# Optimization experiments

Hardware: AMD Instinct MI355X
Metric: run time of the kernel (lower is better)

The kernel has to match this reference:

```python
import jax, jax.numpy as jnp
import numpy as np

B, S, D, H, DH, BS, L, R, V, FF = 4, 4096, 768, 12, 64, 64, 2, 3, 50257, 3072
NB = S // BS          # 64 key/query blocks
NSEL = 5 + R          # 2 global + 3 window + R random key blocks per query block


def layer_norm(x, g, b, eps=1e-12):
    m = jnp.mean(x, axis=-1, keepdims=True)
    v = jnp.mean(jnp.square(x - m), axis=-1, keepdims=True)
    return (x - m) * jax.lax.rsqrt(v + eps) * g + b


def setup_inputs() -> dict:
    key = jax.random.key(0)
    ks = iter(jax.random.split(key, 16))
    p = lambda shape: jax.random.normal(next(ks), shape, jnp.float32) * 0.02
    return {
        'input_ids': jax.random.randint(next(ks), (B, S), 0, V, jnp.int32),
        'attention_mask': jnp.ones((B, S), jnp.int32),
        'label': jax.random.randint(next(ks), (B,), 0, 2, jnp.int32),
        'rand_idx': jax.random.randint(next(ks), (NB, R), 0, NB, jnp.int32),
        'emb': p((V, D)), 'pos_emb': p((S, D)),
        'ln_emb_g': jnp.ones((D,)), 'ln_emb_b': jnp.zeros((D,)),
        'Wqkv': p((L, D, 3 * D)), 'bqkv': jnp.zeros((L, 3 * D)),
        'Wo': p((L, D, D)), 'bo': jnp.zeros((L, D)),
        'ln1_g': jnp.ones((L, D)), 'ln1_b': jnp.zeros((L, D)),
        'Wff1': p((L, D, FF)), 'bff1': jnp.zeros((L, FF)),
        'Wff2': p((L, FF, D)), 'bff2': jnp.zeros((L, D)),
        'ln2_g': jnp.ones((L, D)), 'ln2_b': jnp.zeros((L, D)),
        'Wp': p((D, D)), 'bp': jnp.zeros((D,)),
        'Wc': p((D, 2)), 'bc': jnp.zeros((2,)),
    }


def reference(input_ids, attention_mask, label, rand_idx, emb, pos_emb,
              ln_emb_g, ln_emb_b, Wqkv, bqkv, Wo, bo, ln1_g, ln1_b,
              Wff1, bff1, Wff2, bff2, ln2_g, ln2_b, Wp, bp, Wc, bc):
    blk = jnp.arange(NB, dtype=jnp.int32)
    sel = jnp.concatenate([
        jnp.zeros((NB, 1), jnp.int32),
        ((blk - 1) % NB)[:, None], blk[:, None], ((blk + 1) % NB)[:, None],
        jnp.full((NB, 1), NB - 1, jnp.int32),
        rand_idx.astype(jnp.int32),
    ], axis=1)  # [NB, NSEL]

    h = emb[input_ids] + pos_emb[None]                 # [B,S,D]
    h = layer_norm(h, ln_emb_g, ln_emb_b)

    mblk = attention_mask.reshape(B, NB, BS)
    mask_sel = mblk[:, sel].reshape(B, 1, NB, 1, NSEL * BS)  # gathered key mask
    bias = jnp.where(mask_sel > 0, 0.0, -1e9).astype(h.dtype)

    scale = 1.0 / np.sqrt(DH)
    for l in range(L):
        qkv = h @ Wqkv[l] + bqkv[l]
        q, k, v = jnp.split(qkv, 3, axis=-1)
        to_blocks = lambda t: t.reshape(B, NB, BS, H, DH).transpose(0, 3, 1, 2, 4)  # [B,H,NB,BS,DH]
        qb, kb, vb = to_blocks(q), to_blocks(k), to_blocks(v)
        ksel = kb[:, :, sel].reshape(B, H, NB, NSEL * BS, DH)  # gather sparse key blocks
        vsel = vb[:, :, sel].reshape(B, H, NB, NSEL * BS, DH)
        scores = jnp.einsum('bhnqd,bhnkd->bhnqk', qb, ksel) * scale + bias
        attn = jax.nn.softmax(scores, axis=-1)
        ob = jnp.einsum('bhnqk,bhnkd->bhnqd', attn, vsel)
        o = ob.transpose(0, 2, 3, 1, 4).reshape(B, S, D)
        h = layer_norm(h + o @ Wo[l] + bo[l], ln1_g[l], ln1_b[l])
        ff = jax.nn.gelu(h @ Wff1[l] + bff1[l]) @ Wff2[l] + bff2[l]
        h = layer_norm(h + ff, ln2_g[l], ln2_b[l])

    pooled = jnp.tanh(h[:, 0] @ Wp + bp)               # BERT-style pooler on [CLS]
    probs = jax.nn.softmax(pooled @ Wc + bc, axis=1)
    # Faithful to the original: CrossEntropyLoss applied to softmax OUTPUT (double softmax)
    loss = -jnp.mean(jax.nn.log_softmax(probs, axis=1)[jnp.arange(B), label])
    return probs, loss
```

## Files before the change

kernel.cpp:

```cpp
#include <hip/hip_runtime.h>
#include <hip/hip_bf16.h>
#include <stdint.h>


using bf16 = __hip_bfloat16;
typedef __bf16 bf16x8 __attribute__((ext_vector_type(8)));
typedef float f32x4 __attribute__((ext_vector_type(4)));

__device__ __forceinline__ float b2f(bf16 x) { return __bfloat162float(x); }
__device__ __forceinline__ bf16 f2b(float x) { return __float2bfloat16(x); }
__device__ __forceinline__ float ldf(const void* p, size_t i, int flag) {
  return flag ? __bfloat162float(((const bf16*)p)[i]) : ((const float*)p)[i];
}

__device__ __forceinline__ void gld_lds16(const bf16* g, bf16* l) {
  __builtin_amdgcn_global_load_lds((__attribute__((address_space(1))) void*)g,
                                   (__attribute__((address_space(3))) void*)l, 16, 0, 0);
}

__device__ __forceinline__ f32x4 mfma16(bf16x8 a, bf16x8 b, f32x4 c) {
  return __builtin_amdgcn_mfma_f32_16x16x32_bf16(a, b, c, 0, 0, 0);
}

__global__ void probe_kernel(const uint32_t* __restrict__ g, int* __restrict__ flag) {
  if (threadIdx.x == 0) flag[0] = (g[0] == 0x3F803F80u) ? 1 : 0;
}

__global__ __launch_bounds__(256) void transpose_k(const void* __restrict__ in, size_t in_off,
                                                   bf16* __restrict__ out, int K, int N,
                                                   const int* __restrict__ dflag) {
  __shared__ float tile[32][33];
  const int flag = dflag[0];
  const int bx = blockIdx.x * 32;
  const int by = blockIdx.y * 32;
  const int tx = threadIdx.x & 31, ty = threadIdx.x >> 5;
#pragma unroll
  for (int i = 0; i < 32; i += 8)
    tile[ty + i][tx] = ldf(in, in_off + (size_t)(by + ty + i) * N + bx + tx, flag);
  __syncthreads();
#pragma unroll
  for (int i = 0; i < 32; i += 8)
    out[(size_t)(bx + ty + i) * K + by + tx] = f2b(tile[tx][ty + i]);
}

__global__ __launch_bounds__(256) void embed_ln_kernel(
    const int* __restrict__ ids, const void* __restrict__ emb, const void* __restrict__ pos,
    const void* __restrict__ g, const void* __restrict__ bb, bf16* __restrict__ h,
    const int* __restrict__ dflag) {
  __shared__ float red[8];
  const int flag = dflag[0];
  const int tok = blockIdx.x;
  const int tid = threadIdx.x;
  const int s = tok & 4095;
  const size_t id = (size_t)ids[tok];
  float v[3]; float sum = 0.f, sq = 0.f;
#pragma unroll
  for (int i = 0; i < 3; i++) {
    const int d = tid + i * 256;
    v[i] = ldf(emb, id * 768 + d, flag) + ldf(pos, (size_t)s * 768 + d, flag);
    sum += v[i]; sq += v[i] * v[i];
  }
#pragma unroll
  for (int off = 32; off >= 1; off >>= 1) { sum += __shfl_down(sum, off); sq += __shfl_down(sq, off); }
  if ((tid & 63) == 0) { red[(tid >> 6) * 2] = sum; red[(tid >> 6) * 2 + 1] = sq; }
  __syncthreads();
  sum = red[0] + red[2] + red[4] + red[6];
  sq  = red[1] + red[3] + red[5] + red[7];
  const float mean = sum * (1.0f / 768.0f);
  const float var = sq * (1.0f / 768.0f) - mean * mean;
  const float rs = rsqrtf(var + 1e-12f);
  bf16* hr = h + (size_t)tok * 768;
#pragma unroll
  for (int i = 0; i < 3; i++) {
    const int d = tid + i * 256;
    hr[d] = f2b((v[i] - mean) * rs * ldf(g, d, flag) + ldf(bb, d, flag));
  }
}

__global__ __launch_bounds__(256) void add_ln_kernel(
    bf16* __restrict__ h, const bf16* __restrict__ x,
    const void* __restrict__ g, const void* __restrict__ bb, size_t goff,
    const int* __restrict__ dflag) {
  __shared__ float red[8];
  const int flag = dflag[0];
  const int tok = blockIdx.x;
  const int tid = threadIdx.x;
  const size_t base = (size_t)tok * 768;
  float v[3]; float sum = 0.f, sq = 0.f;
#pragma unroll
  for (int i = 0; i < 3; i++) {
    const int d = tid + i * 256;
    v[i] = b2f(h[base + d]) + b2f(x[base + d]);
    sum += v[i]; sq += v[i] * v[i];
  }
#pragma unroll
  for (int off = 32; off >= 1; off >>= 1) { sum += __shfl_down(sum, off); sq += __shfl_down(sq, off); }
  if ((tid & 63) == 0) { red[(tid >> 6) * 2] = sum; red[(tid >> 6) * 2 + 1] = sq; }
  __syncthreads();
  sum = red[0] + red[2] + red[4] + red[6];
  sq  = red[1] + red[3] + red[5] + red[7];
  const float mean = sum * (1.0f / 768.0f);
  const float var = sq * (1.0f / 768.0f) - mean * mean;
  const float rs = rsqrtf(var + 1e-12f);
#pragma unroll
  for (int i = 0; i < 3; i++) {
    const int d = tid + i * 256;
    h[base + d] = f2b((v[i] - mean) * rs * ldf(g, goff + d, flag) + ldf(bb, goff + d, flag));
  }
}

template <int EPI, bool ABLK>
__global__ __launch_bounds__(256) void gemm_bt(
    const bf16* __restrict__ A, const bf16* __restrict__ Bt,
    const void* __restrict__ bias, size_t bias_off, bf16* __restrict__ C,
    int N, int K,
    bf16* __restrict__ qout, bf16* __restrict__ kout, bf16* __restrict__ vout,
    const int* __restrict__ dflag) {
  __shared__ __align__(16) bf16 sA[128 * 32];
  __shared__ __align__(16) bf16 sB[128 * 32];
  const int m0 = blockIdx.x * 128;
  const int n0 = blockIdx.y * 128;
  const int tid = threadIdx.x;
  const int lane = tid & 63;
  const int wv = tid >> 6;
  const int wm = wv >> 1, wn = wv & 1;
  const int col = lane & 15, quad = lane >> 4;

  f32x4 acc[4][4] = {};

  const int sr = tid >> 2;
  const int sc = (tid & 3) * 8;
  const bf16* gA = A + (size_t)(m0 + sr) * K + sc;
  const bf16* gB = Bt + (size_t)(n0 + sr) * K + sc;
  const size_t rstep = (size_t)64 * K;

  size_t cb0 = 0, cb1 = 0;
  if constexpr (ABLK) {
    const int t0 = m0 + sr, t1 = t0 + 64;
    cb0 = (size_t)(t0 >> 12) * 3145728 + ((t0 >> 6) & 63) * 4096 + (t0 & 63) * 64;
    cb1 = (size_t)(t1 >> 12) * 3145728 + ((t1 >> 6) & 63) * 4096 + (t1 & 63) * 64;
  }

  for (int k0 = 0; k0 < K; k0 += 32) {
    const bf16 *pA0, *pA1;
    if constexpr (ABLK) {
      const int c = k0 + sc;
      const int hh = c >> 6, dh = c & 63;
      pA0 = A + cb0 + hh * 262144 + dh;
      pA1 = A + cb1 + hh * 262144 + dh;
    } else {
      pA0 = gA; pA1 = gA + rstep; gA += 32;
    }
    gld_lds16(pA0, sA + tid * 8);
    gld_lds16(pA1, sA + 2048 + tid * 8);
    gld_lds16(gB, sB + tid * 8);
    gld_lds16(gB + rstep, sB + 2048 + tid * 8);
    gB += 32;
    __syncthreads();
    bf16x8 av[4], bv[4];
#pragma unroll
    for (int t = 0; t < 4; t++)
      av[t] = *(const bf16x8*)(sA + (wm * 64 + t * 16 + col) * 32 + quad * 8);
#pragma unroll
    for (int t = 0; t < 4; t++)
      bv[t] = *(const bf16x8*)(sB + (wn * 64 + t * 16 + col) * 32 + quad * 8);
#pragma unroll
    for (int mt = 0; mt < 4; mt++)
#pragma unroll
      for (int nt = 0; nt < 4; nt++)
        acc[mt][nt] = mfma16(av[mt], bv[nt], acc[mt][nt]);
    __syncthreads();
  }

  const int flag = dflag[0];
#pragma unroll
  for (int nt = 0; nt < 4; nt++) {
    const int n = n0 + wn * 64 + nt * 16 + col;
    const float bsv = ldf(bias, bias_off + n, flag);
#pragma unroll
    for (int mt = 0; mt < 4; mt++) {
#pragma unroll
      for (int r = 0; r < 4; r++) {
        const int m = m0 + wm * 64 + mt * 16 + quad * 4 + r;
        float val = acc[mt][nt][r] + bsv;
        if constexpr (EPI == 1) {
          val = 0.5f * val * (1.0f + tanhf(0.7978845608028654f * (val + 0.044715f * val * val * val)));
        }
        if constexpr (EPI == 2) {
          const int part = (n >= 1536) ? 2 : ((n >= 768) ? 1 : 0);
          const int within = n - part * 768;
          const int hh = within >> 6, dh = within & 63;
          const int bb = m >> 12;
          const int nb = (m >> 6) & 63, pos = m & 63;
          const size_t base = (size_t)((bb * 12 + hh) * 64 + nb) * 4096;
          if (part == 0)      qout[base + pos * 64 + dh] = f2b(val);
          else if (part == 1) kout[base + pos * 64 + dh] = f2b(val);
          else                vout[base + dh * 64 + pos] = f2b(val);
        } else {
          C[(size_t)m * N + n] = f2b(val);
        }
      }
    }
  }
}

__global__ __launch_bounds__(256) void attn_kernel(
    const bf16* q, const bf16* __restrict__ kmat, const bf16* __restrict__ vT,
    const int* __restrict__ amask, const int* __restrict__ rand_idx, bf16* o) {
  __shared__ __align__(16) bf16 plds[4][16][32];
  const int idx = blockIdx.x;
  const int nb = idx & 63;
  const int bh = idx >> 6;
  const int bb = bh / 12;
  const int tid = threadIdx.x;
  const int wv = tid >> 6, lane = tid & 63;
  const int col = lane & 15, quad = lane >> 4;

  int sel[8];
  sel[0] = 0; sel[1] = (nb + 63) & 63; sel[2] = nb; sel[3] = (nb + 1) & 63;
  sel[4] = 63;
  sel[5] = rand_idx[nb * 3 + 0];
  sel[6] = rand_idx[nb * 3 + 1];
  sel[7] = rand_idx[nb * 3 + 2];

  const size_t bhbase = (size_t)bh * 64;
  const bf16* qb = q + (bhbase + nb) * 4096;
  const int qrow = wv * 16 + col;
  const bf16x8 aq0 = *(const bf16x8*)(qb + qrow * 64 + quad * 8);
  const bf16x8 aq1 = *(const bf16x8*)(qb + qrow * 64 + 32 + quad * 8);

  float sreg[32][4];
#pragma unroll
  for (int sb = 0; sb < 8; sb++) {
    const bf16* kb = kmat + (bhbase + sel[sb]) * 4096;
    const int* mrow = amask + bb * 4096 + sel[sb] * 64;
#pragma unroll
    for (int c = 0; c < 4; c++) {
      const int kr = c * 16 + col;
      const bf16x8 bk0 = *(const bf16x8*)(kb + kr * 64 + quad * 8);
      const bf16x8 bk1 = *(const bf16x8*)(kb + kr * 64 + 32 + quad * 8);
      f32x4 t = {};
      t = mfma16(aq0, bk0, t);
      t = mfma16(aq1, bk1, t);
      const float bias = (mrow[kr] > 0) ? 0.0f : -1e9f;
      const int ti = sb * 4 + c;
#pragma unroll
      for (int r = 0; r < 4; r++) sreg[ti][r] = t[r] * 0.125f + bias;
    }
  }

  float mx[4] = {-1e30f, -1e30f, -1e30f, -1e30f};
#pragma unroll
  for (int ti = 0; ti < 32; ti++)
#pragma unroll
    for (int r = 0; r < 4; r++) mx[r] = fmaxf(mx[r], sreg[ti][r]);
#pragma unroll
  for (int off = 8; off >= 1; off >>= 1)
#pragma unroll
    for (int r = 0; r < 4; r++) mx[r] = fmaxf(mx[r], __shfl_xor(mx[r], off));

  float sm[4] = {0.f, 0.f, 0.f, 0.f};
#pragma unroll
  for (int ti = 0; ti < 32; ti++)
#pragma unroll
    for (int r = 0; r < 4; r++) {
      const float p = __expf(sreg[ti][r] - mx[r]);
      sreg[ti][r] = p; sm[r] += p;
    }
#pragma unroll
  for (int off = 8; off >= 1; off >>= 1)
#pragma unroll
    for (int r = 0; r < 4; r++) sm[r] += __shfl_xor(sm[r], off);
  float inv[4];
#pragma unroll
  for (int r = 0; r < 4; r++) inv[r] = 1.0f / sm[r];

  f32x4 oacc[4] = {};
#pragma unroll
  for (int kc = 0; kc < 16; kc++) {
    __syncthreads();
#pragma unroll
    for (int j = 0; j < 2; j++)
#pragma unroll
      for (int r = 0; r < 4; r++)
        plds[wv][quad * 4 + r][j * 16 + col] = f2b(sreg[kc * 2 + j][r] * inv[r]);
    __syncthreads();
    const bf16x8 ap = *(const bf16x8*)(&plds[wv][col][quad * 8]);
    const int sb = kc >> 1;
    const int koff = (kc & 1) * 32 + quad * 8;
    const bf16* vb = vT + (bhbase + sel[sb]) * 4096;
#pragma unroll
    for (int nt = 0; nt < 4; nt++) {
      const bf16x8 bvv = *(const bf16x8*)(vb + (nt * 16 + col) * 64 + koff);
      oacc[nt] = mfma16(ap, bvv, oacc[nt]);
    }
  }

  bf16* ob = o + (bhbase + nb) * 4096;
#pragma unroll
  for (int nt = 0; nt < 4; nt++)
#pragma unroll
    for (int r = 0; r < 4; r++)
      ob[(wv * 16 + quad * 4 + r) * 64 + nt * 16 + col] = f2b(oacc[nt][r]);
}

__global__ __launch_bounds__(768) void pooler_kernel(
    const bf16* __restrict__ h, const void* __restrict__ Wp,
    const void* __restrict__ bp, float* __restrict__ pooled,
    const int* __restrict__ dflag) {
  __shared__ float hrow[768];
  const int flag = dflag[0];
  const int bb = blockIdx.x;
  const int j = threadIdx.x;
  hrow[j] = b2f(h[(size_t)bb * 4096 * 768 + j]);
  __syncthreads();
  float acc = 0.0f;
#pragma unroll 8
  for (int d = 0; d < 768; d++) acc += hrow[d] * ldf(Wp, (size_t)d * 768 + j, flag);
  pooled[bb * 768 + j] = tanhf(acc + ldf(bp, j, flag));
}

__global__ __launch_bounds__(256) void cls_kernel(
    const float* __restrict__ pooled, const void* __restrict__ Wc, const void* __restrict__ bc,
    const int* __restrict__ label, void* __restrict__ out, const int* __restrict__ dflag) {
  __shared__ float lsum[8];
  const int flag = dflag[0];
  const int tid = threadIdx.x;
  const int p = tid >> 5, i = tid & 31;
  const int bb = p >> 1, c = p & 1;
  float acc = 0.0f;
  for (int d = i; d < 768; d += 32) acc += pooled[bb * 768 + d] * ldf(Wc, (size_t)d * 2 + c, flag);
#pragma unroll
  for (int off = 16; off >= 1; off >>= 1) acc += __shfl_xor(acc, off);
  if (i == 0) lsum[p] = acc;
  __syncthreads();
  if (tid == 0) {
    float res[9];
    float loss = 0.0f;
    for (int b = 0; b < 4; b++) {
      const float l0 = lsum[b * 2 + 0] + ldf(bc, 0, flag);
      const float l1 = lsum[b * 2 + 1] + ldf(bc, 1, flag);
      const float m = fmaxf(l0, l1);
      const float e0 = expf(l0 - m), e1 = expf(l1 - m);
      const float s = e0 + e1;
      const float p0 = e0 / s, p1 = e1 / s;
      res[b * 2] = p0; res[b * 2 + 1] = p1;
      const float mm = fmaxf(p0, p1);
      const float lse = mm + logf(expf(p0 - mm) + expf(p1 - mm));
      const float chosen = (label[b] == 0) ? p0 : p1;
      loss -= (chosen - lse);
    }
    res[8] = loss * 0.25f;
    if (flag) { bf16* o = (bf16*)out; for (int j = 0; j < 9; j++) o[j] = f2b(res[j]); }
    else      { float* o = (float*)out; for (int j = 0; j < 9; j++) o[j] = res[j]; }
  }
}

extern "C" void kernel_launch(void* const* d_in, const int* in_sizes, int n_in,
                              void* d_out, int out_size, void* d_ws, size_t ws_size,
                              hipStream_t stream) {
  const int* input_ids      = (const int*)d_in[0];
  const int* attention_mask = (const int*)d_in[1];
  const int* label          = (const int*)d_in[2];
  const int* rand_idx       = (const int*)d_in[3];
  const void* emb      = d_in[4];
  const void* pos_emb  = d_in[5];
  const void* ln_emb_g = d_in[6];
  const void* ln_emb_b = d_in[7];
  const void* Wqkv = d_in[8];
  const void* bqkv = d_in[9];
  const void* Wo   = d_in[10];
  const void* bo   = d_in[11];
  const void* ln1_g = d_in[12];
  const void* ln1_b = d_in[13];
  const void* Wff1 = d_in[14];
  const void* bff1 = d_in[15];
  const void* Wff2 = d_in[16];
  const void* bff2 = d_in[17];
  const void* ln2_g = d_in[18];
  const void* ln2_b = d_in[19];
  const void* Wp = d_in[20];
  const void* bp = d_in[21];
  const void* Wc = d_in[22];
  const void* bc = d_in[23];

  bf16* ws = (bf16*)d_ws;
  size_t off = 0;
  int* dflag = (int*)(ws + off); off += 8;
  bf16* WqkvT = ws + off; off += (size_t)2 * 2304 * 768;
  bf16* WoT   = ws + off; off += (size_t)2 * 768 * 768;
  bf16* Wff1T = ws + off; off += (size_t)2 * 3072 * 768;
  bf16* Wff2T = ws + off; off += (size_t)2 * 768 * 3072;
  bf16* hbuf  = ws + off; off += (size_t)16384 * 768;
  bf16* qo    = ws + off; off += (size_t)16384 * 768;
  bf16* kbf   = ws + off; off += (size_t)16384 * 768;
  bf16* vbf   = ws + off; off += (size_t)16384 * 768;
  bf16* xbf   = ws + off; off += (size_t)16384 * 768;
  bf16* a1buf = ws + off; off += (size_t)16384 * 3072;
  float* pooled = (float*)(ws + off); off += 6144;

  dim3 blk(256);

  probe_kernel<<<1, 64, 0, stream>>>((const uint32_t*)ln_emb_g, dflag);

  for (int l = 0; l < 2; l++) {
    transpose_k<<<dim3(72, 24), blk, 0, stream>>>(Wqkv, (size_t)l * 768 * 2304, WqkvT + (size_t)l * 2304 * 768, 768, 2304, dflag);
    transpose_k<<<dim3(24, 24), blk, 0, stream>>>(Wo, (size_t)l * 768 * 768, WoT + (size_t)l * 768 * 768, 768, 768, dflag);
    transpose_k<<<dim3(96, 24), blk, 0, stream>>>(Wff1, (size_t)l * 768 * 3072, Wff1T + (size_t)l * 3072 * 768, 768, 3072, dflag);
    transpose_k<<<dim3(24, 96), blk, 0, stream>>>(Wff2, (size_t)l * 3072 * 768, Wff2T + (size_t)l * 768 * 3072, 3072, 768, dflag);
  }

  embed_ln_kernel<<<16384, blk, 0, stream>>>(input_ids, emb, pos_emb, ln_emb_g, ln_emb_b, hbuf, dflag);

  for (int l = 0; l < 2; l++) {
    gemm_bt<2, false><<<dim3(128, 18), blk, 0, stream>>>(hbuf, WqkvT + (size_t)l * 2304 * 768, bqkv, (size_t)l * 2304,
                                                         nullptr, 2304, 768, qo, kbf, vbf, dflag);
    attn_kernel<<<3072, blk, 0, stream>>>(qo, kbf, vbf, attention_mask, rand_idx, qo);
    gemm_bt<0, true><<<dim3(128, 6), blk, 0, stream>>>(qo, WoT + (size_t)l * 768 * 768, bo, (size_t)l * 768,
                                                       xbf, 768, 768, nullptr, nullptr, nullptr, dflag);
    add_ln_kernel<<<16384, blk, 0, stream>>>(hbuf, xbf, ln1_g, ln1_b, (size_t)l * 768, dflag);
    gemm_bt<1, false><<<dim3(128, 24), blk, 0, stream>>>(hbuf, Wff1T + (size_t)l * 3072 * 768, bff1, (size_t)l * 3072,
                                                         a1buf, 3072, 768, nullptr, nullptr, nullptr, dflag);
    gemm_bt<0, false><<<dim3(128, 6), blk, 0, stream>>>(a1buf, Wff2T + (size_t)l * 768 * 3072, bff2, (size_t)l * 768,
                                                        xbf, 768, 3072, nullptr, nullptr, nullptr, dflag);
    add_ln_kernel<<<16384, blk, 0, stream>>>(hbuf, xbf, ln2_g, ln2_b, (size_t)l * 768, dflag);
  }

  pooler_kernel<<<4, dim3(768), 0, stream>>>(hbuf, Wp, bp, pooled, dflag);
  cls_kernel<<<1, blk, 0, stream>>>(pooled, Wc, bc, label, d_out, dflag);

  (void)in_sizes; (void)n_in; (void)out_size; (void)ws_size;
}
```

Baseline: 1.863 ms.

## Swizzle GEMM LDS layout and stage epilogue through shared memory for vector stores

Applies an XOR-style rotation to the K-chunk placement in LDS so MFMA operand reads hit distinct banks. Reworks the GEMM epilogue to write each 64-row half of the tile into padded shared memory, then emit 16-byte coalesced global stores, including for the QKV-to-block-layout scatter and the transposed V. It also replaces the tanh-based GELU with an equivalent sigmoid/exp form. The cost is extra barriers and a larger shared-memory footprint per block.

```diff
diff --git a/kernel.cpp b/kernel.cpp
--- a/kernel.cpp
+++ b/kernel.cpp
@@ -5,6 +5,7 @@
 
 using bf16 = __hip_bfloat16;
 typedef __bf16 bf16x8 __attribute__((ext_vector_type(8)));
+typedef __bf16 bf16x4 __attribute__((ext_vector_type(4)));
 typedef float f32x4 __attribute__((ext_vector_type(4)));
 
 __device__ __forceinline__ float b2f(bf16 x) { return __bfloat162float(x); }
@@ -20,6 +21,11 @@
 
 __device__ __forceinline__ f32x4 mfma16(bf16x8 a, bf16x8 b, f32x4 c) {
   return __builtin_amdgcn_mfma_f32_16x16x32_bf16(a, b, c, 0, 0, 0);
+}
+
+__device__ __forceinline__ float gelu_f(float x) {
+  const float z = 1.5957691216057308f * (x + 0.044715f * x * x * x);
+  return x / (1.0f + __expf(-z));
 }
 
 __global__ void probe_kernel(const uint32_t* __restrict__ g, int* __restrict__ flag) {
@@ -116,8 +122,9 @@
     int N, int K,
     bf16* __restrict__ qout, bf16* __restrict__ kout, bf16* __restrict__ vout,
     const int* __restrict__ dflag) {
-  __shared__ __align__(16) bf16 sA[128 * 32];
-  __shared__ __align__(16) bf16 sB[128 * 32];
+  __shared__ __align__(16) bf16 smem[9216];
+  bf16* sA = smem;
+  bf16* sB = smem + 4096;
   const int m0 = blockIdx.x * 128;
   const int n0 = blockIdx.y * 128;
   const int tid = threadIdx.x;
@@ -129,7 +136,8 @@
   f32x4 acc[4][4] = {};
 
   const int sr = tid >> 2;
-  const int sc = (tid & 3) * 8;
+  const int kc = ((tid & 3) - ((tid >> 4) & 3)) & 3;
+  const int sc = kc * 8;
   const bf16* gA = A + (size_t)(m0 + sr) * K + sc;
   const bf16* gB = Bt + (size_t)(n0 + sr) * K + sc;
   const size_t rstep = (size_t)64 * K;
@@ -140,6 +148,8 @@
     cb0 = (size_t)(t0 >> 12) * 3145728 + ((t0 >> 6) & 63) * 4096 + (t0 & 63) * 64;
     cb1 = (size_t)(t1 >> 12) * 3145728 + ((t1 >> 6) & 63) * 4096 + (t1 & 63) * 64;
   }
+
+  const int sl = (quad + (col >> 2)) & 3;
 
   for (int k0 = 0; k0 < K; k0 += 32) {
     const bf16 *pA0, *pA1;
@@ -160,10 +170,10 @@
     bf16x8 av[4], bv[4];
 #pragma unroll
     for (int t = 0; t < 4; t++)
-      av[t] = *(const bf16x8*)(sA + (wm * 64 + t * 16 + col) * 32 + quad * 8);
+      av[t] = *(const bf16x8*)(sA + (wm * 64 + t * 16 + col) * 32 + sl * 8);
 #pragma unroll
     for (int t = 0; t < 4; t++)
-      bv[t] = *(const bf16x8*)(sB + (wn * 64 + t * 16 + col) * 32 + quad * 8);
+      bv[t] = *(const bf16x8*)(sB + (wn * 64 + t * 16 + col) * 32 + sl * 8);
 #pragma unroll
     for (int mt = 0; mt < 4; mt++)
 #pragma unroll
@@ -173,31 +183,86 @@
   }
 
   const int flag = dflag[0];
-#pragma unroll
-  for (int nt = 0; nt < 4; nt++) {
-    const int n = n0 + wn * 64 + nt * 16 + col;
-    const float bsv = ldf(bias, bias_off + n, flag);
-#pragma unroll
-    for (int mt = 0; mt < 4; mt++) {
-#pragma unroll
-      for (int r = 0; r < 4; r++) {
-        const int m = m0 + wm * 64 + mt * 16 + quad * 4 + r;
-        float val = acc[mt][nt][r] + bsv;
-        if constexpr (EPI == 1) {
-          val = 0.5f * val * (1.0f + tanhf(0.7978845608028654f * (val + 0.044715f * val * val * val)));
+  float bsv[4];
+#pragma unroll
+  for (int nt = 0; nt < 4; nt++)
+    bsv[nt] = ldf(bias, bias_off + n0 + wn * 64 + nt * 16 + col, flag);
+
+  if constexpr (EPI != 2) {
+    for (int half = 0; half < 2; half++) {
+      __syncthreads();
+      if (wm == half) {
+#pragma unroll
+        for (int nt = 0; nt < 4; nt++)
+#pragma unroll
+          for (int mt = 0; mt < 4; mt++)
+#pragma unroll
+            for (int r = 0; r < 4; r++) {
+              float val = acc[mt][nt][r] + bsv[nt];
+              if constexpr (EPI == 1) val = gelu_f(val);
+              smem[(mt * 16 + quad * 4 + r) * 136 + wn * 64 + nt * 16 + col] = f2b(val);
+            }
+      }
+      __syncthreads();
+#pragma unroll
+      for (int rr = 0; rr < 4; rr++) {
+        const int row = rr * 16 + (tid >> 4);
+        const int ch = tid & 15;
+        const bf16x8 vv = *(const bf16x8*)(smem + row * 136 + ch * 8);
+        *(bf16x8*)(C + (size_t)(m0 + half * 64 + row) * N + n0 + ch * 8) = vv;
+      }
+    }
+  } else {
+    const int part = (n0 >= 1536) ? 2 : ((n0 >= 768) ? 1 : 0);
+    const int w0 = n0 - part * 768;
+    const int h0 = w0 >> 6;
+    const int bb = m0 >> 12;
+    for (int half = 0; half < 2; half++) {
+      const int nb_ = ((m0 >> 6) & 63) + half;
+      __syncthreads();
+      if (wm == half) {
+        if (part < 2) {
+#pragma unroll
+          for (int nt = 0; nt < 4; nt++)
+#pragma unroll
+            for (int mt = 0; mt < 4; mt++)
+#pragma unroll
+              for (int r = 0; r < 4; r++)
+                smem[(mt * 16 + quad * 4 + r) * 136 + wn * 64 + nt * 16 + col] =
+                    f2b(acc[mt][nt][r] + bsv[nt]);
+        } else {
+#pragma unroll
+          for (int nt = 0; nt < 4; nt++) {
+            const int ncol = wn * 64 + nt * 16 + col;
+#pragma unroll
+            for (int mt = 0; mt < 4; mt++) {
+              bf16x4 pk;
+#pragma unroll
+              for (int r = 0; r < 4; r++) pk[r] = f2b(acc[mt][nt][r] + bsv[nt]);
+              *(bf16x4*)(smem + ncol * 72 + mt * 16 + quad * 4) = pk;
+            }
+          }
         }
-        if constexpr (EPI == 2) {
-          const int part = (n >= 1536) ? 2 : ((n >= 768) ? 1 : 0);
-          const int within = n - part * 768;
-          const int hh = within >> 6, dh = within & 63;
-          const int bb = m >> 12;
-          const int nb = (m >> 6) & 63, pos = m & 63;
-          const size_t base = (size_t)((bb * 12 + hh) * 64 + nb) * 4096;
-          if (part == 0)      qout[base + pos * 64 + dh] = f2b(val);
-          else if (part == 1) kout[base + pos * 64 + dh] = f2b(val);
-          else                vout[base + dh * 64 + pos] = f2b(val);
-        } else {
-          C[(size_t)m * N + n] = f2b(val);
+      }
+      __syncthreads();
+      const int j = tid >> 7;
+      const size_t dbase = (size_t)((bb * 12 + h0 + j) * 64 + nb_) * 4096;
+      if (part < 2) {
+        bf16* dst = (part == 0) ? qout : kout;
+#pragma unroll
+        for (int rr = 0; rr < 4; rr++) {
+          const int tsk = (tid & 127) + rr * 128;
+          const int row = tsk >> 3, pc = tsk & 7;
+          const bf16x8 vv = *(const bf16x8*)(smem + row * 136 + j * 64 + pc * 8);
+          *(bf16x8*)(dst + dbase + row * 64 + pc * 8) = vv;
+        }
+      } else {
+#pragma unroll
+        for (int rr = 0; rr < 4; rr++) {
+          const int tsk = (tid & 127) + rr * 128;
+          const int dh = tsk >> 3, pc = tsk & 7;
+          const bf16x8 vv = *(const bf16x8*)(smem + (j * 64 + dh) * 72 + pc * 8);
+          *(bf16x8*)(vout + dbase + dh * 64 + pc * 8) = vv;
         }
       }
     }
```

Result: faster. 1.790 ms (-3.9%).
